# Kernel optimization log

Measured on AMD Instinct MI355X. Metric: run time of the kernel, lower is better.

Reference implementation:

```python
import jax, jax.numpy as jnp
import numpy as np

N, E, G = 8000, 128000, 4
C, NLM, NL = 64, 16, 4
NEL, NB, NH = 10, 8, 64
RMAX = 5.0
PCUT = 5.0
AVG_NEIGH = 16.0
SIGMA = 1.0
LBOX = 6.0
KR = 3
T = 2
LMAP = jnp.array([0, 1, 1, 1, 2, 2, 2, 2, 2, 3, 3, 3, 3, 3, 3, 3])


def _nvec():
    r = np.arange(-KR, KR + 1)
    n = np.stack(np.meshgrid(r, r, r, indexing='ij'), -1).reshape(-1, 3)
    n = n[np.any(n != 0, axis=1)]  # [342,3], k=0 excluded
    return jnp.asarray(n, jnp.float32)


def sph_harm(u):
    # component-normalized real spherical harmonics up to l=3, unit input u [E,3]
    x, y, z = u[:, 0], u[:, 1], u[:, 2]
    one = jnp.ones_like(x)
    c3, c5, c15 = 3.0 ** 0.5, 5.0 ** 0.5, 15.0 ** 0.5
    Y = [one,
         c3 * x, c3 * y, c3 * z,
         c15 * x * y, c15 * y * z, 0.5 * c5 * (3 * z * z - 1.0), c15 * x * z, 0.5 * c15 * (x * x - y * y),
         (35.0 / 8.0) ** 0.5 * y * (3 * x * x - y * y), 105.0 ** 0.5 * x * y * z,
         (21.0 / 8.0) ** 0.5 * y * (5 * z * z - 1.0), 0.5 * 7.0 ** 0.5 * z * (5 * z * z - 3.0),
         (21.0 / 8.0) ** 0.5 * x * (5 * z * z - 1.0), 0.5 * 105.0 ** 0.5 * z * (x * x - y * y),
         (35.0 / 8.0) ** 0.5 * x * (x * x - 3 * y * y)]
    return jnp.stack(Y, -1)  # [E,16]


def radial_basis(r):
    # Bessel basis * polynomial cutoff (MACE RadialEmbeddingBlock)
    u = r / RMAX
    n = jnp.arange(1, NB + 1, dtype=jnp.float32)
    bes = (2.0 / RMAX) ** 0.5 * jnp.sin(n[None, :] * jnp.pi * u[:, None]) / (r[:, None] + 1e-9)
    p = PCUT
    fc = 1.0 - 0.5 * (p + 1) * (p + 2) * u ** p + p * (p + 2) * u ** (p + 1) - 0.5 * p * (p + 1) * u ** (p + 2)
    fc = fc * (u < 1.0)
    return bes * fc[:, None]  # [E,8]


def setup_inputs() -> dict:
    key = jax.random.key(0)
    ks = jax.random.split(key, 24)

    def p(k, shape, fan_in):
        return jax.random.normal(k, shape, jnp.float32) / (fan_in ** 0.5)

    elem = jax.random.randint(ks[0], (N,), 0, NEL)
    inp = {
        'node_attrs': jax.nn.one_hot(elem, NEL, dtype=jnp.float32),
        'positions': jax.random.uniform(ks[1], (N, 3), jnp.float32) * LBOX,
        'shifts': jnp.zeros((E, 3), jnp.float32),
        'density_coefficients': jax.random.normal(ks[2], (N, 1), jnp.float32) * 0.1,
        'cell': jnp.tile(jnp.eye(3, dtype=jnp.float32) * LBOX, (G, 1, 1)),
        'rcell': jnp.tile(jnp.eye(3, dtype=jnp.float32) / LBOX, (G, 1, 1)),
        'volume': jnp.full((G,), LBOX ** 3, jnp.float32),
        'edge_index': jax.random.randint(ks[3], (2, E), 0, N),
        'batch': jnp.repeat(jnp.arange(G), N // G),
        'emb_W': p(ks[4], (NEL, C), NEL),
        'q_coef': p(ks[5], (T, C), 1),
        'rad_W1': p(ks[6], (T, NB, NH), NB),
        'rad_W2': p(ks[7], (T, NH, NH), NH),
        'rad_W3': p(ks[8], (T, NH, NH), NH),
        'rad_W4': p(ks[9], (T, NH, C * NL), NH),
        'lin_up': p(ks[10], (T, NL, C, C), C),
        'lin_out': p(ks[11], (T, NL, C, C), C),
        'W_sc': p(ks[12], (T, NEL, C, C), C),
        'Wp': p(ks[13], (T, 3, C, C), C),
        'W_read0': p(ks[14], (C,), C),
        'Wread1_a': p(ks[15], (C, 16), C),
        'Wread1_b': p(ks[16], (16,), 16),
        'Wq_read': p(ks[17], (T, C), C),
        'atomic_E': jax.random.normal(ks[18], (NEL,), jnp.float32),
    }
    return inp


def reference(node_attrs, positions, shifts, density_coefficients, cell, rcell, volume,
              edge_index, batch, emb_W, q_coef, rad_W1, rad_W2, rad_W3, rad_W4,
              lin_up, lin_out, W_sc, Wp, W_read0, Wread1_a, Wread1_b, Wq_read, atomic_E):
    sender, receiver = edge_index[0], edge_index[1]
    vec = positions[receiver] - positions[sender] + shifts
    r = jnp.linalg.norm(vec, axis=-1)
    Y = sph_harm(vec / (r[:, None] + 1e-9))      # [E,16]
    ef = radial_basis(r)                          # [E,8]

    q = density_coefficients                      # [N,1], max_l=0 multipoles
    feats = jnp.zeros((N, C, NLM), jnp.float32).at[:, :, 0].set(node_attrs @ emb_W)
    e0 = jax.ops.segment_sum(node_attrs @ atomic_E, batch, G)
    energies = [e0]

    for t in range(T):
        # charge-coefficient injection (charge_coefs_linears)
        feats = feats.at[:, :, 0].add(q * q_coef[t][None, :])
        # per-l linear up
        h = jnp.einsum('ncl,lcd->ndl', feats, lin_up[t][LMAP])
        # radial MLP -> per-edge, per-channel, per-l tensor-product weights
        w = jax.nn.silu(ef @ rad_W1[t])
        w = jax.nn.silu(w @ rad_W2[t])
        w = jax.nn.silu(w @ rad_W3[t])
        w = (w @ rad_W4[t]).reshape(E, C, NL)[:, :, LMAP]   # [E,C,16]
        # depthwise equivariant TP message: gather -> contract -> modulate
        hj = h[sender]                                       # [E,C,16]
        s_e = jnp.einsum('ecl,el->ec', hj, Y)                # edge invariant
        m = w * (Y[:, None, :] * s_e[:, :, None])            # [E,C,16]
        A = jax.ops.segment_sum(m, receiver, N) / AVG_NEIGH  # scatter-reduce
        A = jnp.einsum('ncl,lcd->ndl', A, lin_out[t][LMAP])
        # element-dependent residual (self-connection)
        wn = jnp.einsum('nk,kcd->ncd', node_attrs, W_sc[t])
        sc = jnp.einsum('ncd,ncl->ndl', wn, feats)
        # product block: correlation-3 symmetric-contraction surrogate
        s1 = jnp.sum(A * A, axis=2)                           # [N,C]
        out = (jnp.einsum('ncl,cd->ndl', A, Wp[t, 0])
               + jnp.einsum('ncl,cd->ndl', A * s1[:, :, None], Wp[t, 1])
               + jnp.einsum('ncl,cd->ndl', A * (s1 * s1)[:, :, None], Wp[t, 2]))
        feats = out + sc
        # readout
        if t == T - 1:
            node_e = jax.nn.silu(feats[:, :, 0] @ Wread1_a) @ Wread1_b
        else:
            node_e = feats[:, :, 0] @ W_read0
        node_e = node_e + q[:, 0] * (feats[:, :, 0] @ Wq_read[t])
        energies.append(jax.ops.segment_sum(node_e, batch, G))

    # k-space (Ewald-like) electrostatics with Gaussian-smeared charges
    nv = _nvec()                                              # [K,3]
    kvec = 2.0 * jnp.pi * jnp.einsum('kj,gji->gki', nv, rcell)  # [G,K,3]
    k2 = jnp.sum(kvec * kvec, -1)                             # [G,K]
    phase = jnp.einsum('ni,nki->nk', positions, kvec[batch])  # [N,K]
    Sr = jax.ops.segment_sum(q * jnp.cos(phase), batch, G)
    Si = jax.ops.segment_sum(q * jnp.sin(phase), batch, G)
    filt = jnp.exp(-0.5 * SIGMA * SIGMA * k2) / k2
    Ees = (2.0 * jnp.pi / volume) * jnp.sum(filt * (Sr * Sr + Si * Si), axis=1)

    total_energy = jnp.sum(jnp.stack(energies, -1), -1) + Ees
    total_charge = jax.ops.segment_sum(q[:, 0], batch, G)
    dipole = jax.ops.segment_sum(q * positions, batch, G)
    return total_energy, total_charge, dipole
```

## Files before the change

kernel.cpp:

```cpp
#include <hip/hip_runtime.h>
#include <hip/hip_bf16.h>

constexpr int N    = 8000;
constexpr int E    = 128000;
constexpr int G    = 4;
constexpr int NEL  = 10;
constexpr int NGR  = N / G;
constexpr int NC   = N * 64;
constexpr int NK   = 342;
constexpr float RMAX = 5.0f;
constexpr int HS = 72;
constexpr int WT_T = 25088;

typedef __bf16 bf16x8 __attribute__((ext_vector_type(8)));
typedef float  f32x4v __attribute__((ext_vector_type(4)));
typedef unsigned short u16x8 __attribute__((ext_vector_type(8)));

__device__ __forceinline__ int lmap_rt(int l) { return (l >= 1) + (l >= 4) + (l >= 9); }
__device__ __forceinline__ float silu(float x) { return x / (1.f + __expf(-x)); }
__device__ __forceinline__ float bf2f(unsigned short u) { return __uint_as_float(((unsigned)u) << 16); }
__device__ __forceinline__ unsigned short f2bf(float f) {
    __hip_bfloat16 h = __float2bfloat16(f);
    return *(unsigned short*)&h;
}

__device__ __forceinline__ void mfma_stage(const unsigned short* hsrc, const unsigned short* wt,
                                           int m0, int lane, f32x4v acc[4], bool k8only)
{
    const int quad = lane >> 4;
    const int idx  = lane & 15;
    bf16x8 bz;
    #pragma unroll
    for (int i = 0; i < 8; ++i) bz[i] = (__bf16)0.f;
    bf16x8 a0 = bz, a1 = bz;
    const int mrow = m0 + idx;
    if (k8only) {
        if (quad == 0) a0 = *(const bf16x8*)&hsrc[mrow * HS];
    } else {
        a0 = *(const bf16x8*)&hsrc[mrow * HS + (quad << 3)];
        a1 = *(const bf16x8*)&hsrc[mrow * HS + 32 + (quad << 3)];
    }
    #pragma unroll
    for (int c4 = 0; c4 < 4; ++c4) {
        const int nrow = (c4 << 4) + idx;
        if (k8only) {
            bf16x8 b0 = bz;
            if (quad == 0) b0 = *(const bf16x8*)&wt[nrow * HS];
            acc[c4] = __builtin_amdgcn_mfma_f32_16x16x32_bf16(a0, b0, acc[c4], 0, 0, 0);
        } else {
            const bf16x8 b0 = *(const bf16x8*)&wt[nrow * HS + (quad << 3)];
            const bf16x8 b1 = *(const bf16x8*)&wt[nrow * HS + 32 + (quad << 3)];
            acc[c4] = __builtin_amdgcn_mfma_f32_16x16x32_bf16(a0, b0, acc[c4], 0, 0, 0);
            acc[c4] = __builtin_amdgcn_mfma_f32_16x16x32_bf16(a1, b1, acc[c4], 0, 0, 0);
        }
    }
}

__global__ __launch_bounds__(256) void k_init(const float* __restrict__ na,
    const float* __restrict__ q, const float* __restrict__ pos,
    const int* __restrict__ batch, const float* __restrict__ aE,
    int* __restrict__ elem, float* __restrict__ acc)
{
    __shared__ float s[G * 5];
    if (threadIdx.x < G * 5) s[threadIdx.x] = 0.f;
    __syncthreads();
    const int n = blockIdx.x * 256 + threadIdx.x;
    if (n < N) {
        int el = 0; float best = na[n * NEL];
        #pragma unroll
        for (int j = 1; j < NEL; ++j) { float v = na[n * NEL + j]; if (v > best) { best = v; el = j; } }
        elem[n] = el;
        const int g = batch[n];
        const float qn = q[n];
        atomicAdd(&s[g * 5 + 0], aE[el]);
        atomicAdd(&s[g * 5 + 1], qn);
        atomicAdd(&s[g * 5 + 2], qn * pos[n * 3 + 0]);
        atomicAdd(&s[g * 5 + 3], qn * pos[n * 3 + 1]);
        atomicAdd(&s[g * 5 + 4], qn * pos[n * 3 + 2]);
    }
    __syncthreads();
    if (threadIdx.x < G * 5) atomicAdd(&acc[threadIdx.x], s[threadIdx.x]);
}

__global__ __launch_bounds__(256) void k_feat0(const int* __restrict__ elem,
    const float* __restrict__ embW, float* __restrict__ F)
{
    const int i = blockIdx.x * 256 + threadIdx.x;
    if (i < NC) F[i] = embW[elem[i >> 6] * 64 + (i & 63)];
}

__global__ __launch_bounds__(256) void k_pre(const float* __restrict__ q,
    const float* __restrict__ qc, float* __restrict__ F)
{
    const int i = blockIdx.x * 256 + threadIdx.x;
    if (i < NC) F[i] += q[i >> 6] * qc[i & 63];
}

__global__ __launch_bounds__(256) void k_hist(const int* __restrict__ elem, int* __restrict__ counts)
{
    const int n = blockIdx.x * 256 + threadIdx.x;
    if (n < N) atomicAdd(&counts[elem[n]], 1);
}
__global__ void k_offs(const int* __restrict__ counts, int* __restrict__ offs)
{
    if (threadIdx.x == 0 && blockIdx.x == 0) {
        int o = 0;
        for (int j = 0; j < NEL; ++j) { offs[j] = o; o += (counts[j] + 63) & ~63; }
        offs[NEL] = o;
    }
}
__global__ __launch_bounds__(256) void k_scatter(const int* __restrict__ elem,
    const int* __restrict__ offs, int* __restrict__ cursor, int* __restrict__ perm)
{
    const int n = blockIdx.x * 256 + threadIdx.x;
    if (n < N) {
        const int el = elem[n];
        const int p = atomicAdd(&cursor[el], 1);
        perm[offs[el] + p] = n;
    }
}

__global__ __launch_bounds__(256) void k_gcnt(const int* __restrict__ ei, int* __restrict__ cnt)
{
    const int e = blockIdx.x * 256 + threadIdx.x;
    if (e < E) atomicAdd(&cnt[ei[E + e]], 1);
}
__global__ __launch_bounds__(1024) void k_goff(const int* __restrict__ cnt, int* __restrict__ roff)
{
    __shared__ int part[1024];
    const int t = threadIdx.x;
    const int base = t * 8;
    int loc[8];
    int s = 0;
    #pragma unroll
    for (int i = 0; i < 8; ++i) { loc[i] = s; s += (base + i < N) ? cnt[base + i] : 0; }
    part[t] = s;
    __syncthreads();
    for (int d = 1; d < 1024; d <<= 1) {
        const int v = (t >= d) ? part[t - d] : 0;
        __syncthreads();
        part[t] += v;
        __syncthreads();
    }
    const int excl = (t == 0) ? 0 : part[t - 1];
    #pragma unroll
    for (int i = 0; i < 8; ++i) if (base + i < N) roff[base + i] = excl + loc[i];
    if (t == 0) roff[N] = E;
}
__global__ __launch_bounds__(256) void k_gscat(const int* __restrict__ ei,
    const int* __restrict__ roff, int* __restrict__ cur, int* __restrict__ elist)
{
    const int e = blockIdx.x * 256 + threadIdx.x;
    if (e < E) {
        const int rv = ei[E + e];
        const int p = atomicAdd(&cur[rv], 1);
        elist[roff[rv] + p] = e;
    }
}

__global__ __launch_bounds__(256) void k_geom(const float* __restrict__ pos,
    const float* __restrict__ shifts, const int* __restrict__ ei,
    const int* __restrict__ elist, float4* __restrict__ geomv, int* __restrict__ spck)
{
    const int j = blockIdx.x * 256 + threadIdx.x;
    if (j >= E) return;
    const int e = elist[j];
    const int s = ei[e], rv = ei[E + e];
    const float dx = pos[rv * 3 + 0] - pos[s * 3 + 0] + shifts[e * 3 + 0];
    const float dy = pos[rv * 3 + 1] - pos[s * 3 + 1] + shifts[e * 3 + 1];
    const float dz = pos[rv * 3 + 2] - pos[s * 3 + 2] + shifts[e * 3 + 2];
    const float r = sqrtf(dx * dx + dy * dy + dz * dz);
    const float inv = 1.f / (r + 1e-9f);
    float4 g;
    g.x = dx * inv; g.y = dy * inv; g.z = dz * inv; g.w = r;
    geomv[j] = g;
    spck[j] = s;
}

__global__ __launch_bounds__(256) void k_wprep(const float* __restrict__ rW1,
    const float* __restrict__ rW2, const float* __restrict__ rW3,
    const float* __restrict__ rW4, unsigned short* __restrict__ WT)
{
    const int idx = blockIdx.x * 256 + threadIdx.x;
    if (idx >= 2 * WT_T) return;
    const int t = idx / WT_T;
    const int r = idx % WT_T;
    float v;
    if (r < 512) {
        const int n = r >> 3, k = r & 7;
        v = rW1[t * 512 + k * 64 + n];
    } else if (r < 4608) {
        const int i = r - 512, n = i >> 6, k = i & 63;
        v = rW2[t * 4096 + k * 64 + n];
    } else if (r < 8704) {
        const int i = r - 4608, n = i >> 6, k = i & 63;
        v = rW3[t * 4096 + k * 64 + n];
    } else {
        const int i = r - 8704, n = i >> 6, k = i & 63;
        v = rW4[t * 16384 + k * 256 + n];
    }
    WT[idx] = f2bf(v);
}

__global__ __launch_bounds__(256) void k_wprep2(const float* __restrict__ Wp,
    unsigned short* __restrict__ WpT)
{
    const int idx = blockIdx.x * 256 + threadIdx.x;
    if (idx >= 24576) return;
    const int tp = idx / 4096;
    const int i  = idx % 4096;
    const int d = i >> 6, c = i & 63;
    WpT[idx] = f2bf(Wp[(size_t)tp * 4096 + c * 64 + d]);
}

__global__ __launch_bounds__(256) void k_wprep3(const float* __restrict__ lup,
    const float* __restrict__ lout, const float* __restrict__ Wsc,
    unsigned short* __restrict__ WlupT, unsigned short* __restrict__ WloutT,
    unsigned short* __restrict__ WscT)
{
    const int idx = blockIdx.x * 256 + threadIdx.x;
    if (idx < 32768) {
        const int i = idx & 4095, d = i >> 6, c = i & 63;
        WlupT[idx] = f2bf(lup[(idx >> 12) * 4096 + c * 64 + d]);
    } else if (idx < 65536) {
        const int r = idx - 32768;
        const int i = r & 4095, d = i >> 6, c = i & 63;
        WloutT[r] = f2bf(lout[(r >> 12) * 4096 + c * 64 + d]);
    } else if (idx < 147456) {
        const int r = idx - 65536;
        const int i = r & 4095, d = i >> 6, c = i & 63;
        WscT[r] = f2bf(Wsc[(r >> 12) * 4096 + c * 64 + d]);
    }
}

__global__ __launch_bounds__(256) void k_lgemm_hb(const float* __restrict__ X,
    const unsigned short* __restrict__ WT, unsigned short* __restrict__ Hb)
{
    __shared__ unsigned short Xb[64 * HS];
    __shared__ unsigned short Wt[64 * HS];
    const int l  = blockIdx.y;
    const int nb = blockIdx.x << 6;
    const int t  = threadIdx.x;
    const int lane = t & 63;
    const int m0   = (t >> 6) << 4;
    const int quad = lane >> 4;
    const int idx  = lane & 15;
    const int prow = t >> 2, pkb = (t & 3) << 4;
    const float* Xp = X + (size_t)l * NC + (size_t)nb * 64;
    #pragma unroll
    for (int k = 0; k < 16; ++k) {
        const int i = t + (k << 8);
        Xb[(i >> 6) * HS + (i & 63)] = f2bf(Xp[i]);
    }
    const unsigned short* W = WT + lmap_rt(l) * 4096;
    *(u16x8*)&Wt[prow * HS + pkb]     = *(const u16x8*)&W[prow * 64 + pkb];
    *(u16x8*)&Wt[prow * HS + pkb + 8] = *(const u16x8*)&W[prow * 64 + pkb + 8];
    __syncthreads();
    f32x4v acc[4];
    #pragma unroll
    for (int c = 0; c < 4; ++c) { acc[c][0] = 0.f; acc[c][1] = 0.f; acc[c][2] = 0.f; acc[c][3] = 0.f; }
    mfma_stage(Xb, Wt, m0, lane, acc, false);
    #pragma unroll
    for (int c4 = 0; c4 < 4; ++c4) {
        #pragma unroll
        for (int r = 0; r < 4; ++r) {
            const int n = nb + m0 + (quad << 2) + r;
            const int col = (c4 << 4) + idx;
            Hb[(size_t)n * 1024 + (l << 6) + col] = f2bf(acc[c4][r]);
        }
    }
}

__global__ __launch_bounds__(256) void k_lgemm(const float* __restrict__ X,
    const unsigned short* __restrict__ WT, float* __restrict__ Out)
{
    __shared__ unsigned short Xb[64 * HS];
    __shared__ unsigned short Wt[64 * HS];
    const int l  = blockIdx.y;
    const int nb = blockIdx.x << 6;
    const int t  = threadIdx.x;
    const int lane = t & 63;
    const int m0   = (t >> 6) << 4;
    const int quad = lane >> 4;
    const int idx  = lane & 15;
    const int prow = t >> 2, pkb = (t & 3) << 4;
    const float* Xp = X + (size_t)l * NC + (size_t)nb * 64;
    #pragma unroll
    for (int k = 0; k < 16; ++k) {
        const int i = t + (k << 8);
        Xb[(i >> 6) * HS + (i & 63)] = f2bf(Xp[i]);
    }
    const unsigned short* W = WT + lmap_rt(l) * 4096;
    *(u16x8*)&Wt[prow * HS + pkb]     = *(const u16x8*)&W[prow * 64 + pkb];
    *(u16x8*)&Wt[prow * HS + pkb + 8] = *(const u16x8*)&W[prow * 64 + pkb + 8];
    __syncthreads();
    f32x4v acc[4];
    #pragma unroll
    for (int c = 0; c < 4; ++c) { acc[c][0] = 0.f; acc[c][1] = 0.f; acc[c][2] = 0.f; acc[c][3] = 0.f; }
    mfma_stage(Xb, Wt, m0, lane, acc, false);
    float* Op = Out + (size_t)l * NC + (size_t)nb * 64;
    #pragma unroll
    for (int c4 = 0; c4 < 4; ++c4) {
        #pragma unroll
        for (int r = 0; r < 4; ++r) {
            const int row = m0 + (quad << 2) + r;
            Op[(row << 6) + (c4 << 4) + idx] = acc[c4][r];
        }
    }
}

__global__ __launch_bounds__(256) void k_sc(const float* __restrict__ F,
    const unsigned short* __restrict__ WscT, const int* __restrict__ perm,
    const int* __restrict__ elem, float* __restrict__ Out)
{
    __shared__ unsigned short Xb[64 * HS];
    __shared__ unsigned short Wt[64 * HS];
    __shared__ int rows[64];
    const int l  = blockIdx.y;
    const int tb = blockIdx.x << 6;
    const int t  = threadIdx.x;
    if (t < 64) rows[t] = perm[tb + t];
    __syncthreads();
    if (rows[0] < 0) return;
    const int lane = t & 63;
    const int m0   = (t >> 6) << 4;
    const int quad = lane >> 4;
    const int idx  = lane & 15;
    const int prow = t >> 2, pkb = (t & 3) << 4;
    const unsigned short* W = WscT + elem[rows[0]] * 4096;
    *(u16x8*)&Wt[prow * HS + pkb]     = *(const u16x8*)&W[prow * 64 + pkb];
    *(u16x8*)&Wt[prow * HS + pkb + 8] = *(const u16x8*)&W[prow * 64 + pkb + 8];
    #pragma unroll
    for (int k = 0; k < 16; ++k) {
        const int i = t + (k << 8);
        const int rr = i >> 6, cc = i & 63;
        const int n = rows[rr];
        Xb[rr * HS + cc] = (n >= 0) ? f2bf(F[(size_t)l * NC + (size_t)n * 64 + cc]) : (unsigned short)0;
    }
    __syncthreads();
    f32x4v acc[4];
    #pragma unroll
    for (int c = 0; c < 4; ++c) { acc[c][0] = 0.f; acc[c][1] = 0.f; acc[c][2] = 0.f; acc[c][3] = 0.f; }
    mfma_stage(Xb, Wt, m0, lane, acc, false);
    #pragma unroll
    for (int c4 = 0; c4 < 4; ++c4) {
        #pragma unroll
        for (int r = 0; r < 4; ++r) {
            const int n = rows[m0 + (quad << 2) + r];
            if (n >= 0) Out[(size_t)l * NC + (size_t)n * 64 + (c4 << 4) + idx] = acc[c4][r];
        }
    }
}

__global__ __launch_bounds__(256) void k_wgemm(const float4* __restrict__ geomv,
    const unsigned short* __restrict__ WT, unsigned short* __restrict__ wout)
{
    __shared__ unsigned short hbf[64 * HS];
    __shared__ unsigned short wtb[2][64 * HS];
    __shared__ unsigned short outS[64 * HS];
    const int t = threadIdx.x;
    const int lane = t & 63;
    const int wid  = t >> 6;
    const int m0   = wid << 4;
    const int quad = lane >> 4;
    const int idx  = lane & 15;
    const int j0 = blockIdx.x << 6;
    if (t < 64) {
        const float r = geomv[j0 + t].w;
        const float u  = r * 0.2f;
        const float u2 = u * u, u5 = u2 * u2 * u;
        const float fc = 1.f - 21.f * u5 + 35.f * u5 * u - 15.f * u5 * u2;
        float pref = 0.63245553f * fc / (r + 1e-9f);
        if (u >= 1.f) pref = 0.f;
        const float piu = 3.14159265358979f * u;
        #pragma unroll
        for (int b = 0; b < 8; ++b) hbf[t * HS + b] = f2bf(__sinf((float)(b + 1) * piu) * pref);
    }
    {
        const int n = t >> 2, k = (t & 3) << 1;
        wtb[0][n * HS + k]     = WT[n * 8 + k];
        wtb[0][n * HS + k + 1] = WT[n * 8 + k + 1];
    }
    const int prow = t >> 2, pkb = (t & 3) << 4;
    u16x8 pf0, pf1;
    pf0 = *(const u16x8*)&WT[512 + prow * 64 + pkb];
    pf1 = *(const u16x8*)&WT[512 + prow * 64 + pkb + 8];
    __syncthreads();
    f32x4v acc[4];
    #pragma unroll
    for (int c = 0; c < 4; ++c) { acc[c][0] = 0.f; acc[c][1] = 0.f; acc[c][2] = 0.f; acc[c][3] = 0.f; }
    mfma_stage(hbf, wtb[0], m0, lane, acc, true);
    __syncthreads();
    #pragma unroll
    for (int c4 = 0; c4 < 4; ++c4)
        #pragma unroll
        for (int r = 0; r < 4; ++r)
            hbf[(m0 + (quad << 2) + r) * HS + (c4 << 4) + idx] = f2bf(silu(acc[c4][r]));
    *(u16x8*)&wtb[1][prow * HS + pkb]     = pf0;
    *(u16x8*)&wtb[1][prow * HS + pkb + 8] = pf1;
    pf0 = *(const u16x8*)&WT[4608 + prow * 64 + pkb];
    pf1 = *(const u16x8*)&WT[4608 + prow * 64 + pkb + 8];
    __syncthreads();
    #pragma unroll
    for (int c = 0; c < 4; ++c) { acc[c][0] = 0.f; acc[c][1] = 0.f; acc[c][2] = 0.f; acc[c][3] = 0.f; }
    mfma_stage(hbf, wtb[1], m0, lane, acc, false);
    __syncthreads();
    #pragma unroll
    for (int c4 = 0; c4 < 4; ++c4)
        #pragma unroll
        for (int r = 0; r < 4; ++r)
            hbf[(m0 + (quad << 2) + r) * HS + (c4 << 4) + idx] = f2bf(silu(acc[c4][r]));
    *(u16x8*)&wtb[0][prow * HS + pkb]     = pf0;
    *(u16x8*)&wtb[0][prow * HS + pkb + 8] = pf1;
    pf0 = *(const u16x8*)&WT[8704 + prow * 64 + pkb];
    pf1 = *(const u16x8*)&WT[8704 + prow * 64 + pkb + 8];
    __syncthreads();
    #pragma unroll
    for (int c = 0; c < 4; ++c) { acc[c][0] = 0.f; acc[c][1] = 0.f; acc[c][2] = 0.f; acc[c][3] = 0.f; }
    mfma_stage(hbf, wtb[0], m0, lane, acc, false);
    __syncthreads();
    #pragma unroll
    for (int c4 = 0; c4 < 4; ++c4)
        #pragma unroll
        for (int r = 0; r < 4; ++r)
            hbf[(m0 + (quad << 2) + r) * HS + (c4 << 4) + idx] = f2bf(silu(acc[c4][r]));
    *(u16x8*)&wtb[1][prow * HS + pkb]     = pf0;
    *(u16x8*)&wtb[1][prow * HS + pkb + 8] = pf1;
    pf0 = *(const u16x8*)&WT[8704 + 4096 + prow * 64 + pkb];
    pf1 = *(const u16x8*)&WT[8704 + 4096 + prow * 64 + pkb + 8];
    __syncthreads();
    int cur = 1;
    for (int c = 0; c < 4; ++c) {
        #pragma unroll
        for (int cc = 0; cc < 4; ++cc) { acc[cc][0] = 0.f; acc[cc][1] = 0.f; acc[cc][2] = 0.f; acc[cc][3] = 0.f; }
        mfma_stage(hbf, wtb[cur], m0, lane, acc, false);
        __syncthreads();
        #pragma unroll
        for (int c4 = 0; c4 < 4; ++c4)
            #pragma unroll
            for (int r = 0; r < 4; ++r)
                outS[(m0 + (quad << 2) + r) * HS + (c4 << 4) + idx] = f2bf(acc[c4][r]);
        if (c < 3) {
            *(u16x8*)&wtb[1 - cur][prow * HS + pkb]     = pf0;
            *(u16x8*)&wtb[1 - cur][prow * HS + pkb + 8] = pf1;
            if (c < 2) {
                pf0 = *(const u16x8*)&WT[8704 + (c + 2) * 4096 + prow * 64 + pkb];
                pf1 = *(const u16x8*)&WT[8704 + (c + 2) * 4096 + prow * 64 + pkb + 8];
            }
        }
        __syncthreads();
        *(u16x8*)&wout[(size_t)(j0 + prow) * 256 + (c << 6) + pkb]     = *(const u16x8*)&outS[prow * HS + pkb];
        *(u16x8*)&wout[(size_t)(j0 + prow) * 256 + (c << 6) + pkb + 8] = *(const u16x8*)&outS[prow * HS + pkb + 8];
        cur ^= 1;
    }
}

__global__ __launch_bounds__(256) void k_agg(const float4* __restrict__ geomv,
    const int* __restrict__ spck,
    const unsigned short* __restrict__ Hb, const unsigned short* __restrict__ wb,
    const int* __restrict__ roff, float* __restrict__ A)
{
    const int lane = threadIdx.x & 63;
    const int n = (blockIdx.x << 2) + (threadIdx.x >> 6);
    const int ja = roff[n], jb2 = roff[n + 1];
    float accv[16];
    #pragma unroll
    for (int l = 0; l < 16; ++l) accv[l] = 0.f;
    constexpr int LM[16] = {0,1,1,1,2,2,2,2,2,3,3,3,3,3,3,3};
    if (ja < jb2) {
        const int jlast = jb2 - 1;
        int j1c = ja + 1 < jlast ? ja + 1 : jlast;
        int j2c = ja + 2 < jlast ? ja + 2 : jlast;
        float4 g0 = geomv[ja],  g1 = geomv[j1c],  g2 = geomv[j2c];
        ushort4 w0 = *(const ushort4*)&wb[(size_t)ja * 256 + (lane << 2)];
        ushort4 w1 = *(const ushort4*)&wb[(size_t)j1c * 256 + (lane << 2)];
        ushort4 w2 = *(const ushort4*)&wb[(size_t)j2c * 256 + (lane << 2)];
        int sB = spck[j1c], sC = spck[j2c];
        unsigned short hv[16];
        {
            const int s0 = spck[ja];
            #pragma unroll
            for (int l = 0; l < 16; ++l) hv[l] = Hb[(size_t)s0 * 1024 + (l << 6) + lane];
        }
        for (int j = ja; j < jb2; ++j) {
            const float4 gc = g0;
            const ushort4 wc = w0;
            float hc[16];
            #pragma unroll
            for (int l = 0; l < 16; ++l) hc[l] = bf2f(hv[l]);
            g0 = g1; g1 = g2; w0 = w1; w1 = w2;
            const int sA = sB; sB = sC;
            #pragma unroll
            for (int l = 0; l < 16; ++l) hv[l] = Hb[(size_t)sA * 1024 + (l << 6) + lane];
            const int j3 = j + 3 < jlast ? j + 3 : jlast;
            g2 = geomv[j3];
            w2 = *(const ushort4*)&wb[(size_t)j3 * 256 + (lane << 2)];
            sC = spck[j3];
            if (gc.w < RMAX) {
                const float x = gc.x, y = gc.y, z = gc.z;
                const float xx = x * x, yy = y * y, zz = z * z;
                float Y[16];
                Y[0] = 1.f;
                Y[1] = 1.7320508f * x;  Y[2] = 1.7320508f * y;  Y[3] = 1.7320508f * z;
                Y[4] = 3.8729833f * x * y;  Y[5] = 3.8729833f * y * z;
                Y[6] = 0.5f * 2.2360680f * (3.f * zz - 1.f);
                Y[7] = 3.8729833f * x * z;  Y[8] = 0.5f * 3.8729833f * (xx - yy);
                Y[9]  = 2.0916500f * y * (3.f * xx - yy);
                Y[10] = 10.2469508f * x * y * z;
                Y[11] = 1.6201852f * y * (5.f * zz - 1.f);
                Y[12] = 0.5f * 2.6457513f * z * (5.f * zz - 3.f);
                Y[13] = 1.6201852f * x * (5.f * zz - 1.f);
                Y[14] = 0.5f * 10.2469508f * z * (xx - yy);
                Y[15] = 2.0916500f * x * (xx - 3.f * yy);
                float se = 0.f;
                #pragma unroll
                for (int l = 0; l < 16; ++l) se += hc[l] * Y[l];
                se *= 0.0625f;
                const float wl[4] = { bf2f(wc.x) * se, bf2f(wc.y) * se, bf2f(wc.z) * se, bf2f(wc.w) * se };
                #pragma unroll
                for (int l = 0; l < 16; ++l) accv[l] += wl[LM[l]] * Y[l];
            }
        }
    }
    float* Ap = A + (size_t)n * 64 + lane;
    #pragma unroll
    for (int l = 0; l < 16; ++l) Ap[(size_t)l * NC] = accv[l];
}

__global__ __launch_bounds__(256) void k_s1(const float* __restrict__ H, float* __restrict__ s1)
{
    const int i = blockIdx.x * 256 + threadIdx.x;
    if (i < NC) {
        float s = 0.f;
        #pragma unroll
        for (int l = 0; l < 16; ++l) { const float a = H[(size_t)l * NC + i]; s += a * a; }
        s1[i] = s;
    }
}

__global__ __launch_bounds__(256) void k_out(const float* __restrict__ Ap,
    const float* __restrict__ s1, const unsigned short* __restrict__ WpT,
    const float* __restrict__ sc, float* __restrict__ F)
{
    __shared__ unsigned short Xb[64 * HS];
    __shared__ unsigned short Wt[64 * HS];
    const int l  = blockIdx.y;
    const int nb = blockIdx.x << 6;
    const int t  = threadIdx.x;
    const int lane = t & 63;
    const int m0   = (t >> 6) << 4;
    const int quad = lane >> 4;
    const int idx  = lane & 15;
    const int prow = t >> 2, pkb = (t & 3) << 4;
    const float* Xp = Ap + (size_t)l * NC + (size_t)nb * 64;
    float av[16], sv[16];
    #pragma unroll
    for (int k = 0; k < 16; ++k) {
        const int i = t + (k << 8);
        av[k] = Xp[i];
        sv[k] = s1[nb * 64 + i];
    }
    f32x4v acc[4];
    #pragma unroll
    for (int c = 0; c < 4; ++c) { acc[c][0] = 0.f; acc[c][1] = 0.f; acc[c][2] = 0.f; acc[c][3] = 0.f; }
    for (int p = 0; p < 3; ++p) {
        #pragma unroll
        for (int k = 0; k < 16; ++k) {
            const int i = t + (k << 8);
            Xb[(i >> 6) * HS + (i & 63)] = f2bf(av[k]);
            av[k] *= sv[k];
        }
        *(u16x8*)&Wt[prow * HS + pkb]     = *(const u16x8*)&WpT[p * 4096 + prow * 64 + pkb];
        *(u16x8*)&Wt[prow * HS + pkb + 8] = *(const u16x8*)&WpT[p * 4096 + prow * 64 + pkb + 8];
        __syncthreads();
        mfma_stage(Xb, Wt, m0, lane, acc, false);
        __syncthreads();
    }
    #pragma unroll
    for (int c4 = 0; c4 < 4; ++c4) {
        #pragma unroll
        for (int r = 0; r < 4; ++r) {
            const int row = m0 + (quad << 2) + r;
            const int col = (c4 << 4) + idx;
            const size_t id = (size_t)l * NC + (size_t)(nb + row) * 64 + col;
            F[id] = acc[c4][r] + sc[id];
        }
    }
}

__global__ __launch_bounds__(256) void k_read(const float* __restrict__ F,
    const float* __restrict__ q, const int* __restrict__ batch,
    const float* __restrict__ Wr0, const float* __restrict__ Wa,
    const float* __restrict__ Wb, const float* __restrict__ Wq,
    float* __restrict__ acc, int last)
{
    __shared__ float sred[G];
    if (threadIdx.x < G) sred[threadIdx.x] = 0.f;
    __syncthreads();
    const int n = blockIdx.x * 256 + threadIdx.x;
    if (n < N) {
        float a16[16];
        #pragma unroll
        for (int j = 0; j < 16; ++j) a16[j] = 0.f;
        float ar = 0.f, aq = 0.f;
        const float* f = F + (size_t)n * 64;
        for (int c = 0; c < 64; ++c) {
            const float fv = f[c];
            aq += fv * Wq[c];
            if (last) {
                #pragma unroll
                for (int j = 0; j < 16; ++j) a16[j] += fv * Wa[c * 16 + j];
            } else ar += fv * Wr0[c];
        }
        float en;
        if (last) {
            en = 0.f;
            #pragma unroll
            for (int j = 0; j < 16; ++j) en += silu(a16[j]) * Wb[j];
        } else en = ar;
        en += q[n] * aq;
        atomicAdd(&sred[batch[n]], en);
    }
    __syncthreads();
    if (threadIdx.x < G) atomicAdd(&acc[threadIdx.x * 5], sred[threadIdx.x]);
}

__global__ __launch_bounds__(256) void k_kvec(const float* __restrict__ rcell,
    float* __restrict__ kvec, float* __restrict__ k2)
{
    const int idx = blockIdx.x * 256 + threadIdx.x;
    if (idx >= G * NK) return;
    const int g = idx / NK, k = idx % NK;
    const int kk = k + (k >= 171 ? 1 : 0);
    const int a = kk / 49 - 3, b = (kk / 7) % 7 - 3, c = kk % 7 - 3;
    const float* rc = rcell + g * 9;
    float s = 0.f;
    #pragma unroll
    for (int i = 0; i < 3; ++i) {
        const float kv = 6.283185307f * ((float)a * rc[0 + i] + (float)b * rc[3 + i] + (float)c * rc[6 + i]);
        kvec[idx * 3 + i] = kv;
        s += kv * kv;
    }
    k2[idx] = s;
}

__global__ __launch_bounds__(256) void k_phase(const float* __restrict__ pos,
    const float* __restrict__ q, const float* __restrict__ kvec,
    float* __restrict__ Sr, float* __restrict__ Si)
{
    __shared__ float kvs[38 * 3];
    __shared__ float srs[38], sis[38];
    const int g = blockIdx.z, kc = blockIdx.x, ncb = blockIdx.y;
    const int kbase = kc * 38;
    if (threadIdx.x < 38 * 3) kvs[threadIdx.x] = kvec[((size_t)g * NK + kbase) * 3 + threadIdx.x];
    if (threadIdx.x < 38) { srs[threadIdx.x] = 0.f; sis[threadIdx.x] = 0.f; }
    __syncthreads();
    const int t = threadIdx.x;
    float px = 0.f, py = 0.f, pz = 0.f, qn = 0.f;
    if (t < 250) {
        const int n = g * NGR + ncb * 250 + t;
        px = pos[n * 3]; py = pos[n * 3 + 1]; pz = pos[n * 3 + 2]; qn = q[n];
    }
    const int lane = t & 63;
    for (int j = 0; j < 38; ++j) {
        const float ph = px * kvs[j * 3] + py * kvs[j * 3 + 1] + pz * kvs[j * 3 + 2];
        float sv, cv;
        __sincosf(ph, &sv, &cv);
        float vr = qn * cv, vi = qn * sv;
        #pragma unroll
        for (int o = 32; o > 0; o >>= 1) { vr += __shfl_down(vr, o, 64); vi += __shfl_down(vi, o, 64); }
        if (lane == 0) { atomicAdd(&srs[j], vr); atomicAdd(&sis[j], vi); }
    }
    __syncthreads();
    if (t < 38) {
        atomicAdd(&Sr[g * NK + kbase + t], srs[t]);
        atomicAdd(&Si[g * NK + kbase + t], sis[t]);
    }
}

__global__ __launch_bounds__(512) void k_final(const float* __restrict__ k2,
    const float* __restrict__ Sr, const float* __restrict__ Si,
    const float* __restrict__ vol, const float* __restrict__ acc,
    float* __restrict__ out)
{
    __shared__ float red[512];
    const int g = blockIdx.x, t = threadIdx.x;
    float v = 0.f;
    if (t < NK) {
        const float kk = k2[g * NK + t];
        const float sr = Sr[g * NK + t], si = Si[g * NK + t];
        v = __expf(-0.5f * kk) * (sr * sr + si * si) / kk;
    }
    red[t] = v;
    __syncthreads();
    for (int s2 = 256; s2 > 0; s2 >>= 1) {
        if (t < s2) red[t] += red[t + s2];
        __syncthreads();
    }
    if (t == 0) {
        const float Ees = 6.283185307f / vol[g] * red[0];
        out[g]     = acc[g * 5 + 0] + Ees;
        out[4 + g] = acc[g * 5 + 1];
        out[8 + g * 3 + 0] = acc[g * 5 + 2];
        out[8 + g * 3 + 1] = acc[g * 5 + 3];
        out[8 + g * 3 + 2] = acc[g * 5 + 4];
    }
}

extern "C" void kernel_launch(void* const* d_in, const int* in_sizes, int n_in,
                              void* d_out, int out_size, void* d_ws, size_t ws_size,
                              hipStream_t stream)
{
    const float* na    = (const float*)d_in[0];
    const float* pos   = (const float*)d_in[1];
    const float* shif  = (const float*)d_in[2];
    const float* q     = (const float*)d_in[3];
    const float* rcell = (const float*)d_in[5];
    const float* vol   = (const float*)d_in[6];
    const int*   ei    = (const int*)d_in[7];
    const int*   batch = (const int*)d_in[8];
    const float* embW  = (const float*)d_in[9];
    const float* qcoef = (const float*)d_in[10];
    const float* rW1   = (const float*)d_in[11];
    const float* rW2   = (const float*)d_in[12];
    const float* rW3   = (const float*)d_in[13];
    const float* rW4   = (const float*)d_in[14];
    const float* lup   = (const float*)d_in[15];
    const float* lout  = (const float*)d_in[16];
    const float* Wsc   = (const float*)d_in[17];
    const float* Wp    = (const float*)d_in[18];
    const float* Wr0   = (const float*)d_in[19];
    const float* Wa    = (const float*)d_in[20];
    const float* Wb    = (const float*)d_in[21];
    const float* Wq    = (const float*)d_in[22];
    const float* aE    = (const float*)d_in[23];
    float* out = (float*)d_out;

    float* wsf  = (float*)d_ws;
    float* F    = wsf;
    float* A    = F + 8192000;
    float* R    = A + 8192000;
    float* H2   = R;
    unsigned short* Hb = (unsigned short*)R;
    unsigned short* wb = (unsigned short*)(R + 4096000);
    float* s1   = R + 20480000;
    float* kvec = s1 + 512000;
    float* k2   = kvec + 4104;
    float* Sr   = k2 + 1368;
    float* Si   = Sr + 1368;
    float* acc  = Si + 1368;
    int*   elem = (int*)(acc + 32);
    int*   perm = elem + 8000;
    int*   counts = perm + 8640;
    int*   cursor = counts + 16;
    int*   offs   = cursor + 16;
    int*   roff   = offs + 16;
    int*   cnt    = roff + 8001;
    int*   cur    = cnt + 8000;
    int*   elist  = cur + 8000;
    unsigned short* WTb = (unsigned short*)(((uintptr_t)(elist + E) + 31) & ~(uintptr_t)31);
    unsigned short* WpT = WTb + 2 * WT_T;
    float4* geomv = (float4*)(WpT + 24576);
    int*    spck  = (int*)(geomv + E);
    unsigned short* WlupT  = (unsigned short*)(spck + E);
    unsigned short* WloutT = WlupT + 32768;
    unsigned short* WscT   = WloutT + 32768;

    hipMemsetAsync(F, 0, 8192000 * sizeof(float), stream);
    hipMemsetAsync(Sr, 0, (1368 * 2 + 32) * sizeof(float), stream);
    hipMemsetAsync(perm, 0xFF, 8640 * sizeof(int), stream);
    hipMemsetAsync(counts, 0, 32 * sizeof(int), stream);
    hipMemsetAsync(cnt, 0, 16000 * sizeof(int), stream);

    k_init<<<32, 256, 0, stream>>>(na, q, pos, batch, aE, elem, acc);
    k_feat0<<<2000, 256, 0, stream>>>(elem, embW, F);
    k_hist<<<32, 256, 0, stream>>>(elem, counts);
    k_offs<<<1, 64, 0, stream>>>(counts, offs);
    k_scatter<<<32, 256, 0, stream>>>(elem, offs, cursor, perm);
    k_gcnt<<<500, 256, 0, stream>>>(ei, cnt);
    k_goff<<<1, 1024, 0, stream>>>(cnt, roff);
    k_gscat<<<500, 256, 0, stream>>>(ei, roff, cur, elist);
    k_geom<<<500, 256, 0, stream>>>(pos, shif, ei, elist, geomv, spck);
    k_wprep<<<196, 256, 0, stream>>>(rW1, rW2, rW3, rW4, WTb);
    k_wprep2<<<96, 256, 0, stream>>>(Wp, WpT);
    k_wprep3<<<576, 256, 0, stream>>>(lup, lout, Wsc, WlupT, WloutT, WscT);
    k_kvec<<<6, 256, 0, stream>>>(rcell, kvec, k2);
    k_phase<<<dim3(9, 8, G), 256, 0, stream>>>(pos, q, kvec, Sr, Si);

    for (int t = 0; t < 2; ++t) {
        k_pre<<<2000, 256, 0, stream>>>(q, qcoef + t * 64, F);
        k_lgemm_hb<<<dim3(125, 16), 256, 0, stream>>>(F, WlupT + t * 16384, Hb);
        k_wgemm<<<2000, 256, 0, stream>>>(geomv, WTb + t * WT_T, wb);
        k_agg<<<2000, 256, 0, stream>>>(geomv, spck, Hb, wb, roff, A);
        k_lgemm<<<dim3(125, 16), 256, 0, stream>>>(A, WloutT + t * 16384, H2);
        k_s1<<<2000, 256, 0, stream>>>(H2, s1);
        k_sc<<<dim3(135, 16), 256, 0, stream>>>(F, WscT + t * 40960, perm, elem, A);
        k_out<<<dim3(125, 16), 256, 0, stream>>>(H2, s1, WpT + t * 12288, A, F);
        k_read<<<32, 256, 0, stream>>>(F, q, batch, Wr0, Wa, Wb, Wq + t * 64, acc, t == 1);
    }
    k_final<<<G, 512, 0, stream>>>(k2, Sr, Si, vol, acc, out);
}
```

Before: 564.4 us.

## Transpose node features for vectorized gather and fuse prep kernels

Adds a transpose kernel that reorders the per-node bf16 hidden features from l-major to channel-major, so the edge aggregation gathers each sender's 16 spherical components with two 16-byte vector loads instead of 16 scalar loads. Also folds the charge pre-add into the first GEMM's load, the element histogram into the init kernel, and the three weight-prep kernels into one launch. The transpose costs an extra pass over the hidden buffer and uses the A buffer as scratch. The first GEMM's l==0 blocks now write F in place while the other blocks only read their own l slice.

```diff
diff --git a/kernel.cpp b/kernel.cpp
--- a/kernel.cpp
+++ b/kernel.cpp
@@ -59,7 +59,7 @@
 __global__ __launch_bounds__(256) void k_init(const float* __restrict__ na,
     const float* __restrict__ q, const float* __restrict__ pos,
     const int* __restrict__ batch, const float* __restrict__ aE,
-    int* __restrict__ elem, float* __restrict__ acc)
+    int* __restrict__ elem, int* __restrict__ counts, float* __restrict__ acc)
 {
     __shared__ float s[G * 5];
     if (threadIdx.x < G * 5) s[threadIdx.x] = 0.f;
@@ -70,6 +70,7 @@
         #pragma unroll
         for (int j = 1; j < NEL; ++j) { float v = na[n * NEL + j]; if (v > best) { best = v; el = j; } }
         elem[n] = el;
+        atomicAdd(&counts[el], 1);
         const int g = batch[n];
         const float qn = q[n];
         atomicAdd(&s[g * 5 + 0], aE[el]);
@@ -89,18 +90,6 @@
     if (i < NC) F[i] = embW[elem[i >> 6] * 64 + (i & 63)];
 }
 
-__global__ __launch_bounds__(256) void k_pre(const float* __restrict__ q,
-    const float* __restrict__ qc, float* __restrict__ F)
-{
-    const int i = blockIdx.x * 256 + threadIdx.x;
-    if (i < NC) F[i] += q[i >> 6] * qc[i & 63];
-}
-
-__global__ __launch_bounds__(256) void k_hist(const int* __restrict__ elem, int* __restrict__ counts)
-{
-    const int n = blockIdx.x * 256 + threadIdx.x;
-    if (n < N) atomicAdd(&counts[elem[n]], 1);
-}
 __global__ void k_offs(const int* __restrict__ counts, int* __restrict__ offs)
 {
     if (threadIdx.x == 0 && blockIdx.x == 0) {
@@ -177,63 +166,56 @@
     spck[j] = s;
 }
 
-__global__ __launch_bounds__(256) void k_wprep(const float* __restrict__ rW1,
+__global__ __launch_bounds__(256) void k_wprep_all(const float* __restrict__ rW1,
     const float* __restrict__ rW2, const float* __restrict__ rW3,
-    const float* __restrict__ rW4, unsigned short* __restrict__ WT)
-{
-    const int idx = blockIdx.x * 256 + threadIdx.x;
-    if (idx >= 2 * WT_T) return;
-    const int t = idx / WT_T;
-    const int r = idx % WT_T;
-    float v;
-    if (r < 512) {
-        const int n = r >> 3, k = r & 7;
-        v = rW1[t * 512 + k * 64 + n];
-    } else if (r < 4608) {
-        const int i = r - 512, n = i >> 6, k = i & 63;
-        v = rW2[t * 4096 + k * 64 + n];
-    } else if (r < 8704) {
-        const int i = r - 4608, n = i >> 6, k = i & 63;
-        v = rW3[t * 4096 + k * 64 + n];
-    } else {
-        const int i = r - 8704, n = i >> 6, k = i & 63;
-        v = rW4[t * 16384 + k * 256 + n];
-    }
-    WT[idx] = f2bf(v);
-}
-
-__global__ __launch_bounds__(256) void k_wprep2(const float* __restrict__ Wp,
-    unsigned short* __restrict__ WpT)
-{
-    const int idx = blockIdx.x * 256 + threadIdx.x;
-    if (idx >= 24576) return;
-    const int tp = idx / 4096;
-    const int i  = idx % 4096;
-    const int d = i >> 6, c = i & 63;
-    WpT[idx] = f2bf(Wp[(size_t)tp * 4096 + c * 64 + d]);
-}
-
-__global__ __launch_bounds__(256) void k_wprep3(const float* __restrict__ lup,
-    const float* __restrict__ lout, const float* __restrict__ Wsc,
+    const float* __restrict__ rW4, const float* __restrict__ Wp,
+    const float* __restrict__ lup, const float* __restrict__ lout,
+    const float* __restrict__ Wsc,
+    unsigned short* __restrict__ WT, unsigned short* __restrict__ WpT,
     unsigned short* __restrict__ WlupT, unsigned short* __restrict__ WloutT,
     unsigned short* __restrict__ WscT)
 {
-    const int idx = blockIdx.x * 256 + threadIdx.x;
-    if (idx < 32768) {
+    const int gidx = blockIdx.x * 256 + threadIdx.x;
+    if (gidx < 2 * WT_T) {
+        const int t = gidx / WT_T;
+        const int r = gidx % WT_T;
+        float v;
+        if (r < 512) {
+            const int n = r >> 3, k = r & 7;
+            v = rW1[t * 512 + k * 64 + n];
+        } else if (r < 4608) {
+            const int i = r - 512, n = i >> 6, k = i & 63;
+            v = rW2[t * 4096 + k * 64 + n];
+        } else if (r < 8704) {
+            const int i = r - 4608, n = i >> 6, k = i & 63;
+            v = rW3[t * 4096 + k * 64 + n];
+        } else {
+            const int i = r - 8704, n = i >> 6, k = i & 63;
+            v = rW4[t * 16384 + k * 256 + n];
+        }
+        WT[gidx] = f2bf(v);
+    } else if (gidx < 2 * WT_T + 24576) {
+        const int idx = gidx - 2 * WT_T;
+        const int i  = idx & 4095;
+        const int d = i >> 6, c = i & 63;
+        WpT[idx] = f2bf(Wp[(size_t)(idx >> 12) * 4096 + c * 64 + d]);
+    } else if (gidx < 2 * WT_T + 24576 + 32768) {
+        const int idx = gidx - (2 * WT_T + 24576);
         const int i = idx & 4095, d = i >> 6, c = i & 63;
         WlupT[idx] = f2bf(lup[(idx >> 12) * 4096 + c * 64 + d]);
-    } else if (idx < 65536) {
-        const int r = idx - 32768;
-        const int i = r & 4095, d = i >> 6, c = i & 63;
-        WloutT[r] = f2bf(lout[(r >> 12) * 4096 + c * 64 + d]);
-    } else if (idx < 147456) {
-        const int r = idx - 65536;
-        const int i = r & 4095, d = i >> 6, c = i & 63;
-        WscT[r] = f2bf(Wsc[(r >> 12) * 4096 + c * 64 + d]);
-    }
-}
-
-__global__ __launch_bounds__(256) void k_lgemm_hb(const float* __restrict__ X,
+    } else if (gidx < 2 * WT_T + 24576 + 65536) {
+        const int idx = gidx - (2 * WT_T + 24576 + 32768);
+        const int i = idx & 4095, d = i >> 6, c = i & 63;
+        WloutT[idx] = f2bf(lout[(idx >> 12) * 4096 + c * 64 + d]);
+    } else if (gidx < 2 * WT_T + 24576 + 65536 + 81920) {
+        const int idx = gidx - (2 * WT_T + 24576 + 65536);
+        const int i = idx & 4095, d = i >> 6, c = i & 63;
+        WscT[idx] = f2bf(Wsc[(idx >> 12) * 4096 + c * 64 + d]);
+    }
+}
+
+__global__ __launch_bounds__(256) void k_lgemm_hb(float* __restrict__ F,
+    const float* __restrict__ q, const float* __restrict__ qc,
     const unsigned short* __restrict__ WT, unsigned short* __restrict__ Hb)
 {
     __shared__ unsigned short Xb[64 * HS];
@@ -246,11 +228,21 @@
     const int quad = lane >> 4;
     const int idx  = lane & 15;
     const int prow = t >> 2, pkb = (t & 3) << 4;
-    const float* Xp = X + (size_t)l * NC + (size_t)nb * 64;
-    #pragma unroll
-    for (int k = 0; k < 16; ++k) {
-        const int i = t + (k << 8);
-        Xb[(i >> 6) * HS + (i & 63)] = f2bf(Xp[i]);
+    float* Xp = F + (size_t)l * NC + (size_t)nb * 64;
+    if (l == 0) {
+        #pragma unroll
+        for (int k = 0; k < 16; ++k) {
+            const int i = t + (k << 8);
+            float v = Xp[i] + q[nb + (i >> 6)] * qc[i & 63];
+            Xp[i] = v;
+            Xb[(i >> 6) * HS + (i & 63)] = f2bf(v);
+        }
+    } else {
+        #pragma unroll
+        for (int k = 0; k < 16; ++k) {
+            const int i = t + (k << 8);
+            Xb[(i >> 6) * HS + (i & 63)] = f2bf(Xp[i]);
+        }
     }
     const unsigned short* W = WT + lmap_rt(l) * 4096;
     *(u16x8*)&Wt[prow * HS + pkb]     = *(const u16x8*)&W[prow * 64 + pkb];
@@ -269,6 +261,21 @@
             Hb[(size_t)n * 1024 + (l << 6) + col] = f2bf(acc[c4][r]);
         }
     }
+}
+
+__global__ __launch_bounds__(256) void k_hbT(const unsigned short* __restrict__ Hb,
+    unsigned short* __restrict__ HbT)
+{
+    const int n = (blockIdx.x << 2) + (threadIdx.x >> 6);
+    const int c = threadIdx.x & 63;
+    u16x8 a, b;
+    #pragma unroll
+    for (int l = 0; l < 8; ++l) {
+        a[l] = Hb[(size_t)n * 1024 + (l << 6) + c];
+        b[l] = Hb[(size_t)n * 1024 + ((l + 8) << 6) + c];
+    }
+    *(u16x8*)&HbT[(size_t)n * 1024 + c * 16]     = a;
+    *(u16x8*)&HbT[(size_t)n * 1024 + c * 16 + 8] = b;
 }
 
 __global__ __launch_bounds__(256) void k_lgemm(const float* __restrict__ X,
@@ -457,7 +464,7 @@
 
 __global__ __launch_bounds__(256) void k_agg(const float4* __restrict__ geomv,
     const int* __restrict__ spck,
-    const unsigned short* __restrict__ Hb, const unsigned short* __restrict__ wb,
+    const unsigned short* __restrict__ HbT, const unsigned short* __restrict__ wb,
     const int* __restrict__ roff, float* __restrict__ A)
 {
     const int lane = threadIdx.x & 63;
@@ -476,22 +483,22 @@
         ushort4 w1 = *(const ushort4*)&wb[(size_t)j1c * 256 + (lane << 2)];
         ushort4 w2 = *(const ushort4*)&wb[(size_t)j2c * 256 + (lane << 2)];
         int sB = spck[j1c], sC = spck[j2c];
-        unsigned short hv[16];
+        u16x8 hA, hB;
         {
             const int s0 = spck[ja];
-            #pragma unroll
-            for (int l = 0; l < 16; ++l) hv[l] = Hb[(size_t)s0 * 1024 + (l << 6) + lane];
+            hA = *(const u16x8*)&HbT[(size_t)s0 * 1024 + lane * 16];
+            hB = *(const u16x8*)&HbT[(size_t)s0 * 1024 + lane * 16 + 8];
         }
         for (int j = ja; j < jb2; ++j) {
             const float4 gc = g0;
             const ushort4 wc = w0;
             float hc[16];
             #pragma unroll
-            for (int l = 0; l < 16; ++l) hc[l] = bf2f(hv[l]);
+            for (int l = 0; l < 8; ++l) { hc[l] = bf2f(hA[l]); hc[l + 8] = bf2f(hB[l]); }
             g0 = g1; g1 = g2; w0 = w1; w1 = w2;
             const int sA = sB; sB = sC;
-            #pragma unroll
-            for (int l = 0; l < 16; ++l) hv[l] = Hb[(size_t)sA * 1024 + (l << 6) + lane];
+            hA = *(const u16x8*)&HbT[(size_t)sA * 1024 + lane * 16];
+            hB = *(const u16x8*)&HbT[(size_t)sA * 1024 + lane * 16 + 8];
             const int j3 = j + 3 < jlast ? j + 3 : jlast;
             g2 = geomv[j3];
             w2 = *(const ushort4*)&wb[(size_t)j3 * 256 + (lane << 2)];
@@ -741,7 +748,8 @@
     float* A    = F + 8192000;
     float* R    = A + 8192000;
     float* H2   = R;
-    unsigned short* Hb = (unsigned short*)R;
+    unsigned short* Hbtmp = (unsigned short*)A;
+    unsigned short* HbT   = (unsigned short*)R;
     unsigned short* wb = (unsigned short*)(R + 4096000);
     float* s1   = R + 20480000;
     float* kvec = s1 + 512000;
@@ -772,26 +780,24 @@
     hipMemsetAsync(counts, 0, 32 * sizeof(int), stream);
     hipMemsetAsync(cnt, 0, 16000 * sizeof(int), stream);
 
-    k_init<<<32, 256, 0, stream>>>(na, q, pos, batch, aE, elem, acc);
+    k_init<<<32, 256, 0, stream>>>(na, q, pos, batch, aE, elem, counts, acc);
     k_feat0<<<2000, 256, 0, stream>>>(elem, embW, F);
-    k_hist<<<32, 256, 0, stream>>>(elem, counts);
     k_offs<<<1, 64, 0, stream>>>(counts, offs);
     k_scatter<<<32, 256, 0, stream>>>(elem, offs, cursor, perm);
     k_gcnt<<<500, 256, 0, stream>>>(ei, cnt);
     k_goff<<<1, 1024, 0, stream>>>(cnt, roff);
     k_gscat<<<500, 256, 0, stream>>>(ei, roff, cur, elist);
     k_geom<<<500, 256, 0, stream>>>(pos, shif, ei, elist, geomv, spck);
-    k_wprep<<<196, 256, 0, stream>>>(rW1, rW2, rW3, rW4, WTb);
-    k_wprep2<<<96, 256, 0, stream>>>(Wp, WpT);
-    k_wprep3<<<576, 256, 0, stream>>>(lup, lout, Wsc, WlupT, WloutT, WscT);
+    k_wprep_all<<<868, 256, 0, stream>>>(rW1, rW2, rW3, rW4, Wp, lup, lout, Wsc,
+                                         WTb, WpT, WlupT, WloutT, WscT);
     k_kvec<<<6, 256, 0, stream>>>(rcell, kvec, k2);
     k_phase<<<dim3(9, 8, G), 256, 0, stream>>>(pos, q, kvec, Sr, Si);
 
     for (int t = 0; t < 2; ++t) {
-        k_pre<<<2000, 256, 0, stream>>>(q, qcoef + t * 64, F);
-        k_lgemm_hb<<<dim3(125, 16), 256, 0, stream>>>(F, WlupT + t * 16384, Hb);
+        k_lgemm_hb<<<dim3(125, 16), 256, 0, stream>>>(F, q, qcoef + t * 64, WlupT + t * 16384, Hbtmp);
+        k_hbT<<<2000, 256, 0, stream>>>(Hbtmp, HbT);
         k_wgemm<<<2000, 256, 0, stream>>>(geomv, WTb + t * WT_T, wb);
-        k_agg<<<2000, 256, 0, stream>>>(geomv, spck, Hb, wb, roff, A);
+        k_agg<<<2000, 256, 0, stream>>>(geomv, spck, HbT, wb, roff, A);
         k_lgemm<<<dim3(125, 16), 256, 0, stream>>>(A, WloutT + t * 16384, H2);
         k_s1<<<2000, 256, 0, stream>>>(H2, s1);
         k_sc<<<dim3(135, 16), 256, 0, stream>>>(F, WscT + t * 40960, perm, elem, A);
```

After: 573.1 us. About the same (+1.6%).
